# Kernel tuning notes

Measured on AMD Instinct MI355X. Metric: run time of the kernel, lower is better.

The kernel has to match this reference:

```python
import jax, jax.numpy as jnp
import numpy as np

N, E, D_IN, D_H, D_OUT = 50000, 800000, 128, 128, 64


def _glorot(key, shape):
    fan_in, fan_out = shape[1], shape[0]
    lim = (6.0 / (fan_in + fan_out)) ** 0.5
    return jax.random.uniform(key, shape, jnp.float32, -lim, lim)


def setup_inputs() -> dict:
    key = jax.random.key(0)
    ks = jax.random.split(key, 8)
    x = jax.random.normal(ks[0], (N, D_IN), jnp.float32)
    edge_index = jax.random.randint(ks[1], (2, E), 0, N, jnp.int64)
    # SAGEConv layer 1: lin_l (on aggregated neighbors, with bias) and lin_r (root, no bias)
    W1l = _glorot(ks[2], (D_H, D_IN))
    b1 = jnp.zeros((D_H,), jnp.float32)
    W1r = _glorot(ks[3], (D_H, D_IN))
    # SAGEConv layer 2
    W2l = _glorot(ks[4], (D_OUT, D_H))
    b2 = jnp.zeros((D_OUT,), jnp.float32)
    W2r = _glorot(ks[5], (D_OUT, D_H))
    return {"x": x, "edge_index": edge_index, "W1l": W1l, "b1": b1, "W1r": W1r,
            "W2l": W2l, "b2": b2, "W2r": W2r}


def _sage_conv(x, src, dst, inv_deg, Wl, b, Wr):
    # mean-aggregate neighbor features: gather x[src], scatter-sum into dst, divide by degree
    msg_sum = jax.ops.segment_sum(x[src], dst, num_segments=N)  # [N, d]
    agg = msg_sum * inv_deg[:, None]
    return agg @ Wl.T + b + x @ Wr.T


def reference(x, edge_index, W1l, b1, W1r, W2l, b2, W2r):
    src, dst = edge_index[0], edge_index[1]
    deg = jax.ops.segment_sum(jnp.ones((E,), jnp.float32), dst, num_segments=N)
    inv_deg = jnp.where(deg > 0, 1.0 / jnp.maximum(deg, 1.0), 0.0)
    h = _sage_conv(x, src, dst, inv_deg, W1l, b1, W1r)
    h = jax.nn.relu(h)  # dropout is identity in eval mode
    out = _sage_conv(h, src, dst, inv_deg, W2l, b2, W2r)
    return out
```

## Files before the change

### kernel.cpp

```cpp
#include <hip/hip_runtime.h>
#include <hip/hip_bf16.h>

typedef __hip_bfloat16 bf16;
typedef __attribute__((ext_vector_type(8))) short short8;
typedef __attribute__((ext_vector_type(4))) float f32x4;
typedef unsigned short u16;

#define N_NODES 50000
#define NE      800000
#define DIN     128
#define DH      128
#define DOUT    64
#define MTILES  (N_NODES / 16)
#define CAP     64
#define DSTRIDE 32

__device__ __forceinline__ int clamp_node(int s) {
    return min(max(s, 0), N_NODES - 1);
}
__device__ __forceinline__ float b2f(short s) {
    unsigned u = ((unsigned)(unsigned short)s) << 16;
    float f; __builtin_memcpy(&f, &u, 4); return f;
}
__device__ __forceinline__ short f2b(float f) {
    __hip_bfloat16 h = __float2bfloat16(f);
    short s; __builtin_memcpy(&s, &h, 2); return s;
}

__global__ void k_build(const int* __restrict__ src, const int* __restrict__ dst,
                        int* __restrict__ degPad, u16* __restrict__ csrPad,
                        const float* __restrict__ x, __hip_bfloat162* __restrict__ xb2,
                        const float* __restrict__ W1l, const float* __restrict__ W1r,
                        const float* __restrict__ W2l, const float* __restrict__ W2r,
                        bf16* __restrict__ W1b, bf16* __restrict__ W2b) {
    int b = blockIdx.x;
    if (b < 3125) {
        int e = b * 256 + threadIdx.x;
        int t = clamp_node(dst[e]);
        int pos = atomicAdd(&degPad[t * DSTRIDE], 1);
        if (pos < CAP) csrPad[t * CAP + pos] = (u16)src[e];
    } else if (b < 3125 + 6250) {
        int i = (b - 3125) * 256 + threadIdx.x;
        float4 v = ((const float4*)x)[i];
        __hip_bfloat162 a, bb;
        a.x = __float2bfloat16(v.x); a.y = __float2bfloat16(v.y);
        bb.x = __float2bfloat16(v.z); bb.y = __float2bfloat16(v.w);
        xb2[2 * i]     = a;
        xb2[2 * i + 1] = bb;
    } else {
        int i = (b - 9375) * 256 + threadIdx.x;
        if (i < 128 * 256) {
            int n = i >> 8, k = i & 255;
            float v = (k < 128) ? W1l[n * 128 + k] : W1r[n * 128 + (k - 128)];
            W1b[i] = __float2bfloat16(v);
        } else {
            int j = i - 128 * 256;
            int n = j >> 7, k = j & 127;
            float v = (n < 64) ? W2l[n * 128 + k] : W2r[(n - 64) * 128 + k];
            W2b[j] = __float2bfloat16(v);
        }
    }
}

__global__ __launch_bounds__(256) void k_agg1(const int* __restrict__ degPad, const u16* __restrict__ csrPad,
                                              const short* __restrict__ xb,
                                              short* __restrict__ msg) {
    int node = blockIdx.x * 4 + (threadIdx.x >> 6);
    if (node >= N_NODES) return;
    int lane = threadIdx.x & 63;
    int g = lane >> 4, c = lane & 15;
    int d = min(max(degPad[node * DSTRIDE], 0), CAP);
    int lo = node * CAP, hi = lo + d;
    float acc[8];
    #pragma unroll
    for (int j = 0; j < 8; ++j) acc[j] = 0.f;
    int i = lo;
    for (; i + 15 < hi; i += 16) {
        int n0 = clamp_node(csrPad[i + g]);
        int n1 = clamp_node(csrPad[i + 4 + g]);
        int n2 = clamp_node(csrPad[i + 8 + g]);
        int n3 = clamp_node(csrPad[i + 12 + g]);
        short8 v0 = *(const short8*)(xb + (size_t)n0 * DIN + c * 8);
        short8 v1 = *(const short8*)(xb + (size_t)n1 * DIN + c * 8);
        short8 v2 = *(const short8*)(xb + (size_t)n2 * DIN + c * 8);
        short8 v3 = *(const short8*)(xb + (size_t)n3 * DIN + c * 8);
        #pragma unroll
        for (int j = 0; j < 8; ++j)
            acc[j] += (b2f(v0[j]) + b2f(v1[j])) + (b2f(v2[j]) + b2f(v3[j]));
    }
    for (; i + 7 < hi; i += 8) {
        int n0 = clamp_node(csrPad[i + g]);
        int n1 = clamp_node(csrPad[i + 4 + g]);
        short8 v0 = *(const short8*)(xb + (size_t)n0 * DIN + c * 8);
        short8 v1 = *(const short8*)(xb + (size_t)n1 * DIN + c * 8);
        #pragma unroll
        for (int j = 0; j < 8; ++j) acc[j] += b2f(v0[j]) + b2f(v1[j]);
    }
    for (; i < hi; i += 4) {
        bool valid = (i + g) < hi;
        int n = clamp_node(csrPad[valid ? (i + g) : i]);
        short8 v = *(const short8*)(xb + (size_t)n * DIN + c * 8);
        if (valid) {
            #pragma unroll
            for (int j = 0; j < 8; ++j) acc[j] += b2f(v[j]);
        }
    }
    #pragma unroll
    for (int j = 0; j < 8; ++j) {
        acc[j] += __shfl_xor(acc[j], 16);
        acc[j] += __shfl_xor(acc[j], 32);
    }
    if (g == 0) {
        float inv = (d > 0) ? 1.0f / (float)d : 0.0f;
        short8 o;
        #pragma unroll
        for (int j = 0; j < 8; ++j) o[j] = f2b(acc[j] * inv);
        *(short8*)(msg + (size_t)node * DIN + c * 8) = o;
    }
}

__global__ __launch_bounds__(256) void k_mfma12(const short* __restrict__ msg,
                                                const short* __restrict__ xb,
                                                const short* __restrict__ W1b,
                                                const float* __restrict__ b1,
                                                const short* __restrict__ W2b,
                                                bf16* __restrict__ pb,
                                                float* __restrict__ qbuf) {
    __shared__ short hs[16][136];
    int wave = threadIdx.x >> 6, lane = threadIdx.x & 63;
    int q = lane >> 4, mr = lane & 15;
    int n0 = wave * 32;
    short8 Bf1[2][8];
    #pragma unroll
    for (int t = 0; t < 2; ++t) {
        const short* wrow = W1b + (size_t)(n0 + t * 16 + mr) * 256 + q * 8;
        #pragma unroll
        for (int ks = 0; ks < 8; ++ks) Bf1[t][ks] = *(const short8*)(wrow + ks * 32);
    }
    short8 Bf2[2][4];
    #pragma unroll
    for (int t = 0; t < 2; ++t) {
        const short* wrow = W2b + (size_t)(n0 + t * 16 + mr) * 128 + q * 8;
        #pragma unroll
        for (int ks = 0; ks < 4; ++ks) Bf2[t][ks] = *(const short8*)(wrow + ks * 32);
    }
    float bias0 = b1[n0 + mr], bias1 = b1[n0 + 16 + mr];
    for (int mt = blockIdx.x; mt < MTILES; mt += gridDim.x) {
        const short* a0 = msg + (size_t)(mt * 16 + mr) * DIN + q * 8;
        const short* a1 = xb  + (size_t)(mt * 16 + mr) * DIN + q * 8;
        short8 Af[8];
        #pragma unroll
        for (int ks = 0; ks < 4; ++ks) Af[ks]     = *(const short8*)(a0 + ks * 32);
        #pragma unroll
        for (int ks = 0; ks < 4; ++ks) Af[4 + ks] = *(const short8*)(a1 + ks * 32);
        f32x4 acc0 = {0.f, 0.f, 0.f, 0.f}, acc1 = {0.f, 0.f, 0.f, 0.f};
        #pragma unroll
        for (int ks = 0; ks < 8; ++ks) {
            acc0 = __builtin_amdgcn_mfma_f32_16x16x32_bf16(Af[ks], Bf1[0][ks], acc0, 0, 0, 0);
            acc1 = __builtin_amdgcn_mfma_f32_16x16x32_bf16(Af[ks], Bf1[1][ks], acc1, 0, 0, 0);
        }
        __syncthreads();
        #pragma unroll
        for (int r = 0; r < 4; ++r) {
            int row = q * 4 + r;
            float v0 = acc0[r] + bias0;
            float v1 = acc1[r] + bias1;
            hs[row][n0 + mr]      = f2b(v0 > 0.f ? v0 : 0.f);
            hs[row][n0 + 16 + mr] = f2b(v1 > 0.f ? v1 : 0.f);
        }
        __syncthreads();
        short8 Ah[4];
        #pragma unroll
        for (int ks = 0; ks < 4; ++ks) Ah[ks] = *(const short8*)(&hs[mr][ks * 32 + q * 8]);
        f32x4 c20 = {0.f, 0.f, 0.f, 0.f}, c21 = {0.f, 0.f, 0.f, 0.f};
        #pragma unroll
        for (int ks = 0; ks < 4; ++ks) {
            c20 = __builtin_amdgcn_mfma_f32_16x16x32_bf16(Ah[ks], Bf2[0][ks], c20, 0, 0, 0);
            c21 = __builtin_amdgcn_mfma_f32_16x16x32_bf16(Ah[ks], Bf2[1][ks], c21, 0, 0, 0);
        }
        #pragma unroll
        for (int r = 0; r < 4; ++r) {
            int row = mt * 16 + q * 4 + r;
            int c0 = n0 + mr, c1 = n0 + 16 + mr;
            if (c0 < 64) {
                pb[(size_t)row * 64 + c0] = __float2bfloat16(c20[r]);
                pb[(size_t)row * 64 + c1] = __float2bfloat16(c21[r]);
            } else {
                qbuf[(size_t)row * 64 + (c0 - 64)] = c20[r];
                qbuf[(size_t)row * 64 + (c1 - 64)] = c21[r];
            }
        }
    }
}

__global__ __launch_bounds__(256) void k_agg2f(const int* __restrict__ degPad, const u16* __restrict__ csrPad,
                                               const short* __restrict__ pb, const float* __restrict__ qbuf,
                                               const float* __restrict__ b2, float* __restrict__ out) {
    int node = blockIdx.x * 4 + (threadIdx.x >> 6);
    if (node >= N_NODES) return;
    int lane = threadIdx.x & 63;
    int g = lane >> 3, c = lane & 7;
    int d = min(max(degPad[node * DSTRIDE], 0), CAP);
    int lo = node * CAP, hi = lo + d;
    float acc[8];
    #pragma unroll
    for (int j = 0; j < 8; ++j) acc[j] = 0.f;
    int i = lo;
    for (; i + 31 < hi; i += 32) {
        int n0 = clamp_node(csrPad[i + g]);
        int n1 = clamp_node(csrPad[i + 8 + g]);
        int n2 = clamp_node(csrPad[i + 16 + g]);
        int n3 = clamp_node(csrPad[i + 24 + g]);
        short8 v0 = *(const short8*)(pb + (size_t)n0 * 64 + c * 8);
        short8 v1 = *(const short8*)(pb + (size_t)n1 * 64 + c * 8);
        short8 v2 = *(const short8*)(pb + (size_t)n2 * 64 + c * 8);
        short8 v3 = *(const short8*)(pb + (size_t)n3 * 64 + c * 8);
        #pragma unroll
        for (int j = 0; j < 8; ++j)
            acc[j] += (b2f(v0[j]) + b2f(v1[j])) + (b2f(v2[j]) + b2f(v3[j]));
    }
    for (; i + 15 < hi; i += 16) {
        int n0 = clamp_node(csrPad[i + g]);
        int n1 = clamp_node(csrPad[i + 8 + g]);
        short8 v0 = *(const short8*)(pb + (size_t)n0 * 64 + c * 8);
        short8 v1 = *(const short8*)(pb + (size_t)n1 * 64 + c * 8);
        #pragma unroll
        for (int j = 0; j < 8; ++j) acc[j] += b2f(v0[j]) + b2f(v1[j]);
    }
    for (; i < hi; i += 8) {
        bool valid = (i + g) < hi;
        int n = clamp_node(csrPad[valid ? (i + g) : i]);
        short8 v = *(const short8*)(pb + (size_t)n * 64 + c * 8);
        if (valid) {
            #pragma unroll
            for (int j = 0; j < 8; ++j) acc[j] += b2f(v[j]);
        }
    }
    #pragma unroll
    for (int j = 0; j < 8; ++j) {
        acc[j] += __shfl_xor(acc[j], 8);
        acc[j] += __shfl_xor(acc[j], 16);
        acc[j] += __shfl_xor(acc[j], 32);
    }
    if (g == 0) {
        float inv = (d > 0) ? 1.0f / (float)d : 0.0f;
        const float* qr = qbuf + (size_t)node * 64 + c * 8;
        const float* br = b2 + c * 8;
        float* orow = out + (size_t)node * 64 + c * 8;
        float4 o0, o1;
        o0.x = acc[0] * inv + qr[0] + br[0];
        o0.y = acc[1] * inv + qr[1] + br[1];
        o0.z = acc[2] * inv + qr[2] + br[2];
        o0.w = acc[3] * inv + qr[3] + br[3];
        o1.x = acc[4] * inv + qr[4] + br[4];
        o1.y = acc[5] * inv + qr[5] + br[5];
        o1.z = acc[6] * inv + qr[6] + br[6];
        o1.w = acc[7] * inv + qr[7] + br[7];
        ((float4*)orow)[0] = o0;
        ((float4*)orow)[1] = o1;
    }
}

extern "C" void kernel_launch(void* const* d_in, const int* in_sizes, int n_in,
                              void* d_out, int out_size, void* d_ws, size_t ws_size,
                              hipStream_t stream) {
    const float* x   = (const float*)d_in[0];
    const int*   ei  = (const int*)  d_in[1];
    const float* W1l = (const float*)d_in[2];
    const float* b1  = (const float*)d_in[3];
    const float* W1r = (const float*)d_in[4];
    const float* W2l = (const float*)d_in[5];
    const float* b2  = (const float*)d_in[6];
    const float* W2r = (const float*)d_in[7];
    float* out = (float*)d_out;

    const int* src = ei;
    const int* dst = ei + NE;

    char* ws = (char*)d_ws;
    int*   degPad = (int*)  (ws + 0);
    u16*   csrPad = (u16*)  (ws + 6400000);
    short* xb     = (short*)(ws + 12800000);
    short* msg    = (short*)(ws + 25600000);
    bf16*  pb     = (bf16*) (ws + 38400000);
    float* qbuf   = (float*)(ws + 44800000);
    bf16*  W1b    = (bf16*) (ws + 57600000);
    bf16*  W2b    = (bf16*) (ws + 57665536);

    hipMemsetAsync(degPad, 0, 6400000, stream);

    k_build<<<9567, 256, 0, stream>>>(src, dst, degPad, csrPad, x, (__hip_bfloat162*)xb,
                                      W1l, W1r, W2l, W2r, W1b, W2b);
    k_agg1<<<(N_NODES + 3) / 4, 256, 0, stream>>>(degPad, csrPad, xb, msg);
    k_mfma12<<<512, 256, 0, stream>>>(msg, xb, (const short*)W1b, b1, (const short*)W2b, pb, qbuf);
    k_agg2f<<<(N_NODES + 3) / 4, 256, 0, stream>>>(degPad, csrPad, (const short*)pb, qbuf, b2, out);
}
```

Baseline: 202.5 us.

## Partition CSR edge scatter by destination range per XCD

```diff
diff --git a/kernel.cpp b/kernel.cpp
--- a/kernel.cpp
+++ b/kernel.cpp
@@ -14,6 +14,11 @@
 #define MTILES  (N_NODES / 16)
 #define CAP     64
 #define DSTRIDE 32
+#define NXCD    8
+#define NPX     (N_NODES / NXCD)
+#define ECHUNK  2048
+#define NCHUNK  ((NE + ECHUNK - 1) / ECHUNK)
+#define SCAT_BLKS (NCHUNK * NXCD)
 
 __device__ __forceinline__ int clamp_node(int s) {
     return min(max(s, 0), N_NODES - 1);
@@ -34,13 +39,28 @@
                         const float* __restrict__ W2l, const float* __restrict__ W2r,
                         bf16* __restrict__ W1b, bf16* __restrict__ W2b) {
     int b = blockIdx.x;
-    if (b < 3125) {
-        int e = b * 256 + threadIdx.x;
-        int t = clamp_node(dst[e]);
-        int pos = atomicAdd(&degPad[t * DSTRIDE], 1);
-        if (pos < CAP) csrPad[t * CAP + pos] = (u16)src[e];
-    } else if (b < 3125 + 6250) {
-        int i = (b - 3125) * 256 + threadIdx.x;
+    if (b < SCAT_BLKS) {
+        int chunk = b >> 3;
+        int lo = (b & 7) * NPX, hi = lo + NPX;
+        int e0 = chunk * ECHUNK + threadIdx.x * 8;
+        if (e0 + 7 < NE) {
+            int4 d0 = *(const int4*)(dst + e0);
+            int4 d1 = *(const int4*)(dst + e0 + 4);
+            int4 s0 = *(const int4*)(src + e0);
+            int4 s1 = *(const int4*)(src + e0 + 4);
+            int dv[8] = {d0.x, d0.y, d0.z, d0.w, d1.x, d1.y, d1.z, d1.w};
+            int sv[8] = {s0.x, s0.y, s0.z, s0.w, s1.x, s1.y, s1.z, s1.w};
+            #pragma unroll
+            for (int j = 0; j < 8; ++j) {
+                int t = dv[j];
+                if (t >= lo && t < hi) {
+                    int pos = atomicAdd(&degPad[t * DSTRIDE], 1);
+                    if (pos < CAP) csrPad[t * CAP + pos] = (u16)sv[j];
+                }
+            }
+        }
+    } else if (b < SCAT_BLKS + 6250) {
+        int i = (b - SCAT_BLKS) * 256 + threadIdx.x;
         float4 v = ((const float4*)x)[i];
         __hip_bfloat162 a, bb;
         a.x = __float2bfloat16(v.x); a.y = __float2bfloat16(v.y);
@@ -48,7 +68,7 @@
         xb2[2 * i]     = a;
         xb2[2 * i + 1] = bb;
     } else {
-        int i = (b - 9375) * 256 + threadIdx.x;
+        int i = (b - SCAT_BLKS - 6250) * 256 + threadIdx.x;
         if (i < 128 * 256) {
             int n = i >> 8, k = i & 255;
             float v = (k < 128) ? W1l[n * 128 + k] : W1r[n * 128 + (k - 128)];
@@ -289,8 +309,9 @@
 
     hipMemsetAsync(degPad, 0, 6400000, stream);
 
-    k_build<<<9567, 256, 0, stream>>>(src, dst, degPad, csrPad, x, (__hip_bfloat162*)xb,
-                                      W1l, W1r, W2l, W2r, W1b, W2b);
+    k_build<<<SCAT_BLKS + 6250 + 192, 256, 0, stream>>>(src, dst, degPad, csrPad,
+                                                        x, (__hip_bfloat162*)xb,
+                                                        W1l, W1r, W2l, W2r, W1b, W2b);
     k_agg1<<<(N_NODES + 3) / 4, 256, 0, stream>>>(degPad, csrPad, xb, msg);
     k_mfma12<<<512, 256, 0, stream>>>(msg, xb, (const short*)W1b, b1, (const short*)W2b, pb, qbuf);
     k_agg2f<<<(N_NODES + 3) / 4, 256, 0, stream>>>(degPad, csrPad, (const short*)pb, qbuf, b2, out);
```

Result: faster. 195.8 us (-3.3%).
